# Kernel optimization log

Measured on AMD Instinct MI355X. Metric: run time of the kernel, lower is better.

The kernel has to match this reference:

```python
import jax, jax.numpy as jnp
import numpy as np

T, B, I, H = 512, 64, 1024, 1024
G = 4 * H + 1  # 4 LSTM gates + 1 boundary gate (HM-LSTM)
STDV = 1.0 / np.sqrt(H)


def setup_inputs() -> dict:
    key = jax.random.key(0)
    ks = jax.random.split(key, 5)
    u = lambda k, shape: jax.random.uniform(k, shape, jnp.float32, -STDV, STDV)
    return {
        "x": jax.random.normal(ks[0], (T, B, I), jnp.float32),
        "W_ih": u(ks[1], (G, I)),
        "W_hh": u(ks[2], (G, H)),
        "b_ih": u(ks[3], (G,)),
        "b_hh": u(ks[4], (G,)),
    }


def reference(x, W_ih, W_hh, b_ih, b_hh):
    h_dim = W_hh.shape[1]
    # Precompute input contribution for all timesteps in one big GEMM: [T,B,G]
    gx_all = jnp.einsum("tbi,gi->tbg", x, W_ih) + b_ih + b_hh
    Bsz = x.shape[1]
    h0 = jnp.zeros((Bsz, h_dim), x.dtype)
    c0 = jnp.zeros((Bsz, h_dim), x.dtype)

    def step(carry, gx):
        h, c = carry
        g = gx + h @ W_hh.T  # [B, 4H+1]
        i = jax.nn.sigmoid(g[:, :h_dim])
        f = jax.nn.sigmoid(g[:, h_dim:2 * h_dim])
        gg = jnp.tanh(g[:, 2 * h_dim:3 * h_dim])
        o = jax.nn.sigmoid(g[:, 3 * h_dim:4 * h_dim])
        z = jax.nn.sigmoid(g[:, 4 * h_dim:])  # [B,1] boundary gate
        ig = i * gg
        # HM-LSTM soft boundary: FLUSH (c=i*g) when z->1, UPDATE otherwise
        c_new = z * ig + (1.0 - z) * (f * c + ig)
        h_new = o * jnp.tanh(c_new)
        return (h_new, c_new), h_new

    (hT, cT), out = jax.lax.scan(step, (h0, c0), gx_all)
    return out, hT, cT
```

## Files before the change

kernel.cpp:

```cpp
#include <hip/hip_runtime.h>
#include <cstdint>
#include <cstddef>

typedef unsigned short u16;
typedef short bf16x8 __attribute__((ext_vector_type(8)));
typedef u16   u16x8  __attribute__((ext_vector_type(8)));
typedef float f32x4  __attribute__((ext_vector_type(4)));

#define NT  512
#define NB  64
#define NH  1024
#define NTB 32768
#define G4  4096

#define AS1C(p) ((const __attribute__((address_space(1))) void*)(p))
#define AS3(p)  ((__attribute__((address_space(3))) void*)(p))

__device__ __forceinline__ float b2f(u16 u){
  return __uint_as_float(((unsigned)u) << 16);
}
__device__ __forceinline__ u16 f2b(float f){
  unsigned u = __float_as_uint(f);
  return (u16)((u + 0x7fffu + ((u >> 16) & 1u)) >> 16);
}

__global__ void cvt_bf16(const float* __restrict__ in, u16* __restrict__ out, int n8){
  int stride = gridDim.x * blockDim.x;
  for (int i = blockIdx.x * blockDim.x + threadIdx.x; i < n8; i += stride){
    const float4* p = (const float4*)(in + (size_t)i * 8);
    float4 a = p[0], b = p[1];
    u16x8 r;
    r[0]=f2b(a.x); r[1]=f2b(a.y); r[2]=f2b(a.z); r[3]=f2b(a.w);
    r[4]=f2b(b.x); r[5]=f2b(b.y); r[6]=f2b(b.z); r[7]=f2b(b.w);
    *(u16x8*)(out + (size_t)i * 8) = r;
  }
}

__global__ void zpre_kernel(const float* __restrict__ x, const float* __restrict__ Wih,
                            const float* __restrict__ b_ih, const float* __restrict__ b_hh,
                            float* __restrict__ zp){
  int gw   = (blockIdx.x * 256 + threadIdx.x) >> 6;
  int lane = threadIdx.x & 63;
  const float* wz = Wih + (size_t)4096 * 1024;
  float4 wv[4];
  #pragma unroll
  for (int j = 0; j < 4; ++j) wv[j] = *(const float4*)&wz[lane*16 + j*4];
  float bz = b_ih[4096] + b_hh[4096];
  for (int r = gw; r < NTB; r += 1024){
    const float* xr = x + (size_t)r * 1024 + lane * 16;
    float s = 0.f;
    #pragma unroll
    for (int j = 0; j < 4; ++j){
      float4 xv = *(const float4*)&xr[j*4];
      s += xv.x*wv[j].x + xv.y*wv[j].y + xv.z*wv[j].z + xv.w*wv[j].w;
    }
    #pragma unroll
    for (int o = 32; o > 0; o >>= 1) s += __shfl_down(s, o);
    if (lane == 0) zp[r] = s + bz;
  }
}

template<typename GT>
__global__ __launch_bounds__(256, 2) void gemm_gx(
    const u16* __restrict__ Xb, const u16* __restrict__ Wb,
    const float* __restrict__ b_ih, const float* __restrict__ b_hh,
    GT* __restrict__ gx)
{
  __shared__ u16 As[128*32];
  __shared__ u16 Bs[128*32];
  const int tid  = threadIdx.x;
  const int lane = tid & 63, wave = tid >> 6;
  const int wr = wave >> 1, wc = wave & 1;
  const int m0 = (blockIdx.x & 255) * 128;
  const int n0 = (blockIdx.x >> 8) * 128;
  const int srow = wave * 16 + (lane >> 2);
  const int scol = (lane & 3) * 8;
  const u16* gA = Xb + (size_t)(m0 + srow) * 1024 + scol;
  const u16* gB = Wb + (size_t)(n0 + srow) * 1024 + scol;
  char* lA = (char*)As + wave * 1024;
  char* lB = (char*)Bs + wave * 1024;
  const int fr = lane & 15, fo = (lane >> 4) * 8;

  f32x4 acc[4][4] = {};
  for (int k0 = 0; k0 < 1024; k0 += 32){
    __syncthreads();
    __builtin_amdgcn_global_load_lds(AS1C(gA + k0),            AS3(lA),        16, 0, 0);
    __builtin_amdgcn_global_load_lds(AS1C(gA + 64*1024 + k0),  AS3(lA + 4096), 16, 0, 0);
    __builtin_amdgcn_global_load_lds(AS1C(gB + k0),            AS3(lB),        16, 0, 0);
    __builtin_amdgcn_global_load_lds(AS1C(gB + 64*1024 + k0),  AS3(lB + 4096), 16, 0, 0);
    __syncthreads();
    bf16x8 a[4], b[4];
    #pragma unroll
    for (int mi = 0; mi < 4; ++mi)
      a[mi] = *(const bf16x8*)&As[(wr*64 + mi*16 + fr)*32 + fo];
    #pragma unroll
    for (int ni = 0; ni < 4; ++ni)
      b[ni] = *(const bf16x8*)&Bs[(wc*64 + ni*16 + fr)*32 + fo];
    #pragma unroll
    for (int mi = 0; mi < 4; ++mi)
      #pragma unroll
      for (int ni = 0; ni < 4; ++ni)
        acc[mi][ni] = __builtin_amdgcn_mfma_f32_16x16x32_bf16(a[mi], b[ni], acc[mi][ni], 0, 0, 0);
  }
  const int orow = (lane >> 4) * 4, ocol = lane & 15;
  #pragma unroll
  for (int ni = 0; ni < 4; ++ni){
    const int g = n0 + wc*64 + ni*16 + ocol;
    const float bias = b_ih[g] + b_hh[g];
    #pragma unroll
    for (int mi = 0; mi < 4; ++mi){
      const size_t rb = (size_t)(m0 + wr*64 + mi*16 + orow);
      #pragma unroll
      for (int r = 0; r < 4; ++r){
        float v = acc[mi][ni][r] + bias;
        if constexpr (sizeof(GT) == 4)
          __builtin_nontemporal_store(v, (float*)gx + (rb + r)*G4 + g);
        else
          __builtin_nontemporal_store(f2b(v), (u16*)gx + (rb + r)*G4 + g);
      }
    }
  }
}

__device__ __forceinline__ float ld_gx(const float* p){ return __builtin_nontemporal_load(p); }
__device__ __forceinline__ float ld_gx(const u16* p){ return b2f(__builtin_nontemporal_load(p)); }

template<typename GT>
__global__ __launch_bounds__(256, 1) void hmlstm_scan(
    const u16* __restrict__ Whh, const GT* __restrict__ gx,
    const float* __restrict__ zpre, u16* __restrict__ h0, u16* __restrict__ h1,
    float* __restrict__ out, unsigned* __restrict__ bar)
{
  const int tid  = threadIdx.x;
  const int lane = tid & 63, wave = tid >> 6;
  const int wg = blockIdx.x;
  const int mb = wg >> 6, hb = wg & 63;
  const int fr = lane & 15, hi4 = lane >> 4;
  const int b_l = tid >> 4, h_l = tid & 15;
  const int browg = mb*16 + b_l;

  __shared__ u16  hs[16*1024];
  __shared__ float glds[4][16][16];
  __shared__ float zpart[4][16];
  __shared__ u16  wz[1024];

  ((unsigned long long*)wz)[tid] = ((const unsigned long long*)(Whh + (size_t)4096*1024))[tid];

  const int grow = wave*1024 + hb*16 + fr;
  bf16x8 Bw[32];
  #pragma unroll
  for (int kc = 0; kc < 32; ++kc)
    Bw[kc] = *(const bf16x8*)&Whh[(size_t)grow*1024 + kc*32 + hi4*8];
  #pragma unroll
  for (int kc = 0; kc < 32; ++kc)
    asm volatile("" : "+v"(Bw[kc]));

  {
    u16* p = h0 + (size_t)mb*16384 + hb*256 + tid;
    unsigned z = 0;
    asm volatile("global_store_short %0, %1, off sc0 sc1" :: "v"(p), "v"(z) : "memory");
    asm volatile("s_waitcnt vmcnt(0)" ::: "memory");
  }
  __syncthreads();
  unsigned* myflag = bar + mb*64 + hb;
  const unsigned* gflags = bar + mb*64;
  if (tid == 0){
    unsigned one = 1;
    asm volatile("global_store_dword %0, %1, off sc0 sc1" :: "v"(myflag), "v"(one) : "memory");
  }

  float c_reg = 0.f;

  for (int t = 0; t < NT; ++t){
    const u16* hc = (t & 1) ? h1 : h0;
    u16*       hn = (t & 1) ? h0 : h1;

    float gxl[4];
    const GT* gp = gx + ((size_t)t*64 + mb*16 + hi4*4)*G4 + wave*1024 + hb*16 + fr;
    #pragma unroll
    for (int r = 0; r < 4; ++r) gxl[r] = ld_gx(gp + (size_t)r*G4);
    float zpc = zpre[t*64 + browg];

    {
      const unsigned* fp = gflags + lane;
      unsigned fv, tgt = (unsigned)(t + 1);
      do {
        asm volatile("global_load_dword %0, %1, off sc0 sc1\n\ts_waitcnt vmcnt(0)"
                     : "=v"(fv) : "v"(fp) : "memory");
      } while (!__all((int)(fv >= tgt)));
      __builtin_amdgcn_sched_barrier(0);
    }

    uint4 sv[8];
    #pragma unroll
    for (int j = 0; j < 8; ++j){
      int idx = tid + j*256;
      int row = idx >> 7, cc = idx & 127;
      const u16* src = hc + (size_t)(mb*16 + row)*1024 + cc*8;
      asm volatile("global_load_dwordx4 %0, %1, off sc0 sc1" : "=v"(sv[j]) : "v"(src) : "memory");
    }
    asm volatile("s_waitcnt vmcnt(0)" ::: "memory");
    __builtin_amdgcn_sched_barrier(0);
    #pragma unroll
    for (int j = 0; j < 8; ++j){
      int idx = tid + j*256;
      int row = idx >> 7, cc = idx & 127;
      *(uint4*)((char*)hs + row*2048 + ((cc*16) ^ ((row&7)<<4))) = sv[j];
    }
    __syncthreads();

    f32x4 acc[4] = {}, az = {};
    #pragma unroll
    for (int kc = 0; kc < 32; ++kc){
      bf16x8 a = *(const bf16x8*)((char*)hs + fr*2048 + ((kc*64 + hi4*16) ^ ((fr&7)<<4)));
      acc[kc & 3] = __builtin_amdgcn_mfma_f32_16x16x32_bf16(a, Bw[kc], acc[kc & 3], 0, 0, 0);
    }
    #pragma unroll
    for (int q = 0; q < 8; ++q){
      int kcz = wave*8 + q;
      bf16x8 a  = *(const bf16x8*)((char*)hs + fr*2048 + ((kcz*64 + hi4*16) ^ ((fr&7)<<4)));
      bf16x8 bz = *(const bf16x8*)&wz[kcz*32 + hi4*8];
      az = __builtin_amdgcn_mfma_f32_16x16x32_bf16(a, bz, az, 0, 0, 0);
    }
    f32x4 ac = (acc[0] + acc[1]) + (acc[2] + acc[3]);

    #pragma unroll
    for (int r = 0; r < 4; ++r){
      float v = ac[r] + gxl[r];
      float s = (wave == 2) ? (2.f/(1.f + __expf(-2.f*v)) - 1.f)
                            : (1.f/(1.f + __expf(-v)));
      glds[wave][hi4*4 + r][fr] = s;
    }
    if (fr == 0){
      #pragma unroll
      for (int r = 0; r < 4; ++r) zpart[wave][hi4*4 + r] = az[r];
    }
    __syncthreads();

    float iv = glds[0][b_l][h_l], fvg = glds[1][b_l][h_l];
    float gv = glds[2][b_l][h_l], ov = glds[3][b_l][h_l];
    float zs = zpart[0][b_l] + zpart[1][b_l] + zpart[2][b_l] + zpart[3][b_l];
    float zv = 1.f/(1.f + __expf(-(zpc + zs)));
    float ig = iv * gv;
    float cn = zv*ig + (1.f - zv)*(fvg*c_reg + ig);
    float th = 2.f/(1.f + __expf(-2.f*cn)) - 1.f;
    float hv_ = ov * th;
    c_reg = cn;
    const int hoff = browg*1024 + hb*16 + h_l;
    {
      unsigned hv16 = (unsigned)f2b(hv_);
      asm volatile("global_store_short %0, %1, off sc0 sc1" :: "v"(hn + hoff), "v"(hv16) : "memory");
    }
    __builtin_nontemporal_store(hv_, out + (size_t)t*65536 + hoff);
    if (t == NT-1){
      out[(size_t)NT*65536 + hoff] = hv_;
      out[(size_t)NT*65536 + 65536 + hoff] = cn;
    }
    asm volatile("s_waitcnt vmcnt(0)" ::: "memory");
    __syncthreads();
    if (tid == 0){
      unsigned pv = (unsigned)(t + 2);
      asm volatile("global_store_dword %0, %1, off sc0 sc1" :: "v"(myflag), "v"(pv) : "memory");
    }
  }
}

extern "C" void kernel_launch(void* const* d_in, const int* in_sizes, int n_in,
                              void* d_out, int out_size, void* d_ws, size_t ws_size,
                              hipStream_t stream)
{
  (void)in_sizes; (void)n_in; (void)out_size;
  const float* x    = (const float*)d_in[0];
  const float* Wih  = (const float*)d_in[1];
  const float* Whh  = (const float*)d_in[2];
  const float* b_ih = (const float*)d_in[3];
  const float* b_hh = (const float*)d_in[4];
  float* out = (float*)d_out;

  size_t off = 0;
  auto alloc = [&](size_t bytes)->void*{
    void* p = (char*)d_ws + off;
    off = (off + bytes + 255) & ~(size_t)255;
    return p;
  };
  u16*  xb   = (u16*) alloc((size_t)NTB*1024*2);
  u16*  wihb = (u16*) alloc((size_t)4097*1024*2);
  u16*  whhb = (u16*) alloc((size_t)4097*1024*2);
  u16*  hb   = (u16*) alloc((size_t)2*65536*2);
  float* zp  = (float*)alloc((size_t)NTB*4);
  unsigned* bar = (unsigned*)alloc(4096);
  bool g32 = (ws_size >= off + (size_t)NTB*G4*4);
  void* gxp = (char*)d_ws + off;

  hipMemsetAsync(bar, 0, 4096, stream);
  cvt_bf16<<<dim3(2048), dim3(256), 0, stream>>>(x,   xb,   NTB*1024/8);
  cvt_bf16<<<dim3(512),  dim3(256), 0, stream>>>(Wih, wihb, 4097*1024/8);
  cvt_bf16<<<dim3(512),  dim3(256), 0, stream>>>(Whh, whhb, 4097*1024/8);
  zpre_kernel<<<dim3(256), dim3(256), 0, stream>>>(x, Wih, b_ih, b_hh, zp);
  if (g32){
    gemm_gx<float><<<dim3(8192), dim3(256), 0, stream>>>(xb, wihb, b_ih, b_hh, (float*)gxp);
    hmlstm_scan<float><<<dim3(256), dim3(256), 0, stream>>>(whhb, (const float*)gxp, zp,
                                                            hb, hb + 65536, out, bar);
  } else {
    gemm_gx<u16><<<dim3(8192), dim3(256), 0, stream>>>(xb, wihb, b_ih, b_hh, (u16*)gxp);
    hmlstm_scan<u16><<<dim3(256), dim3(256), 0, stream>>>(whhb, (const u16*)gxp, zp,
                                                          hb, hb + 65536, out, bar);
  }
}
```

Measured before the change: 3.274 ms.

## Use per-wave flags, unique h buffers per step, and direct global-to-LDS loads

```diff
diff --git a/kernel.cpp b/kernel.cpp
--- a/kernel.cpp
+++ b/kernel.cpp
@@ -22,6 +22,12 @@
 __device__ __forceinline__ u16 f2b(float f){
   unsigned u = __float_as_uint(f);
   return (u16)((u + 0x7fffu + ((u >> 16) & 1u)) >> 16);
+}
+__device__ __forceinline__ float fsigmoid(float x){
+  return __builtin_amdgcn_rcpf(1.f + __builtin_amdgcn_exp2f(-1.442695041f * x));
+}
+__device__ __forceinline__ float ftanh(float x){
+  return 2.f * __builtin_amdgcn_rcpf(1.f + __builtin_amdgcn_exp2f(-2.885390082f * x)) - 1.f;
 }
 
 __global__ void cvt_bf16(const float* __restrict__ in, u16* __restrict__ out, int n8){
@@ -128,7 +134,7 @@
 template<typename GT>
 __global__ __launch_bounds__(256, 1) void hmlstm_scan(
     const u16* __restrict__ Whh, const GT* __restrict__ gx,
-    const float* __restrict__ zpre, u16* __restrict__ h0, u16* __restrict__ h1,
+    const float* __restrict__ zpre, u16* __restrict__ hbase,
     float* __restrict__ out, unsigned* __restrict__ bar)
 {
   const int tid  = threadIdx.x;
@@ -156,15 +162,14 @@
     asm volatile("" : "+v"(Bw[kc]));
 
   {
-    u16* p = h0 + (size_t)mb*16384 + hb*256 + tid;
+    u16* p = hbase + (size_t)mb*16384 + hb*256 + tid;
     unsigned z = 0;
     asm volatile("global_store_short %0, %1, off sc0 sc1" :: "v"(p), "v"(z) : "memory");
     asm volatile("s_waitcnt vmcnt(0)" ::: "memory");
   }
-  __syncthreads();
-  unsigned* myflag = bar + mb*64 + hb;
-  const unsigned* gflags = bar + mb*64;
-  if (tid == 0){
+  unsigned* myflag = bar + mb*256 + hb*4 + wave;
+  const unsigned* gflags = bar + mb*256;
+  if (lane == 0){
     unsigned one = 1;
     asm volatile("global_store_dword %0, %1, off sc0 sc1" :: "v"(myflag), "v"(one) : "memory");
   }
@@ -172,8 +177,8 @@
   float c_reg = 0.f;
 
   for (int t = 0; t < NT; ++t){
-    const u16* hc = (t & 1) ? h1 : h0;
-    u16*       hn = (t & 1) ? h0 : h1;
+    const u16* hc = hbase + (size_t)t * 65536;
+    u16*       hn = hbase + (size_t)(t + 1) * 65536;
 
     float gxl[4];
     const GT* gp = gx + ((size_t)t*64 + mb*16 + hi4*4)*G4 + wave*1024 + hb*16 + fr;
@@ -182,31 +187,31 @@
     float zpc = zpre[t*64 + browg];
 
     {
-      const unsigned* fp = gflags + lane;
-      unsigned fv, tgt = (unsigned)(t + 1);
+      const unsigned* fp = gflags + lane*4;
+      unsigned tgt = (unsigned)(t + 1);
+      uint4 fv;
+      unsigned mn;
       do {
-        asm volatile("global_load_dword %0, %1, off sc0 sc1\n\ts_waitcnt vmcnt(0)"
+        asm volatile("global_load_dwordx4 %0, %1, off sc0 sc1\n\ts_waitcnt vmcnt(0)"
                      : "=v"(fv) : "v"(fp) : "memory");
-      } while (!__all((int)(fv >= tgt)));
+        mn = min(min(fv.x, fv.y), min(fv.z, fv.w));
+      } while (!__all((int)(mn >= tgt)));
       __builtin_amdgcn_sched_barrier(0);
     }
 
-    uint4 sv[8];
-    #pragma unroll
-    for (int j = 0; j < 8; ++j){
-      int idx = tid + j*256;
-      int row = idx >> 7, cc = idx & 127;
-      const u16* src = hc + (size_t)(mb*16 + row)*1024 + cc*8;
-      asm volatile("global_load_dwordx4 %0, %1, off sc0 sc1" : "=v"(sv[j]) : "v"(src) : "memory");
+    {
+      const char* gsrc = (const char*)hc + (size_t)mb * 32768;
+      char* hsB = (char*)hs;
+      #pragma unroll
+      for (int j = 0; j < 8; ++j){
+        int chunk = wave*8 + j;
+        int row   = chunk >> 1;
+        int srcoff = row*2048 + ((((chunk & 1)*64 + lane)*16) ^ ((row & 7) << 4));
+        __builtin_amdgcn_global_load_lds(AS1C(gsrc + srcoff), AS3(hsB + chunk*1024), 16, 0, 0);
+      }
     }
     asm volatile("s_waitcnt vmcnt(0)" ::: "memory");
     __builtin_amdgcn_sched_barrier(0);
-    #pragma unroll
-    for (int j = 0; j < 8; ++j){
-      int idx = tid + j*256;
-      int row = idx >> 7, cc = idx & 127;
-      *(uint4*)((char*)hs + row*2048 + ((cc*16) ^ ((row&7)<<4))) = sv[j];
-    }
     __syncthreads();
 
     f32x4 acc[4] = {}, az = {};
@@ -227,8 +232,7 @@
     #pragma unroll
     for (int r = 0; r < 4; ++r){
       float v = ac[r] + gxl[r];
-      float s = (wave == 2) ? (2.f/(1.f + __expf(-2.f*v)) - 1.f)
-                            : (1.f/(1.f + __expf(-v)));
+      float s = (wave == 2) ? ftanh(v) : fsigmoid(v);
       glds[wave][hi4*4 + r][fr] = s;
     }
     if (fr == 0){
@@ -240,27 +244,27 @@
     float iv = glds[0][b_l][h_l], fvg = glds[1][b_l][h_l];
     float gv = glds[2][b_l][h_l], ov = glds[3][b_l][h_l];
     float zs = zpart[0][b_l] + zpart[1][b_l] + zpart[2][b_l] + zpart[3][b_l];
-    float zv = 1.f/(1.f + __expf(-(zpc + zs)));
+    float zv = fsigmoid(zpc + zs);
     float ig = iv * gv;
     float cn = zv*ig + (1.f - zv)*(fvg*c_reg + ig);
-    float th = 2.f/(1.f + __expf(-2.f*cn)) - 1.f;
-    float hv_ = ov * th;
+    float hv_ = ov * ftanh(cn);
     c_reg = cn;
     const int hoff = browg*1024 + hb*16 + h_l;
+
     {
       unsigned hv16 = (unsigned)f2b(hv_);
       asm volatile("global_store_short %0, %1, off sc0 sc1" :: "v"(hn + hoff), "v"(hv16) : "memory");
-    }
+      asm volatile("s_waitcnt vmcnt(0)" ::: "memory");
+      if (lane == 0){
+        unsigned pv = (unsigned)(t + 2);
+        asm volatile("global_store_dword %0, %1, off sc0 sc1" :: "v"(myflag), "v"(pv) : "memory");
+      }
+    }
+
     __builtin_nontemporal_store(hv_, out + (size_t)t*65536 + hoff);
     if (t == NT-1){
       out[(size_t)NT*65536 + hoff] = hv_;
       out[(size_t)NT*65536 + 65536 + hoff] = cn;
-    }
-    asm volatile("s_waitcnt vmcnt(0)" ::: "memory");
-    __syncthreads();
-    if (tid == 0){
-      unsigned pv = (unsigned)(t + 2);
-      asm volatile("global_store_dword %0, %1, off sc0 sc1" :: "v"(myflag), "v"(pv) : "memory");
     }
   }
 }
@@ -283,11 +287,11 @@
     off = (off + bytes + 255) & ~(size_t)255;
     return p;
   };
-  u16*  xb   = (u16*) alloc((size_t)NTB*1024*2);
-  u16*  wihb = (u16*) alloc((size_t)4097*1024*2);
-  u16*  whhb = (u16*) alloc((size_t)4097*1024*2);
-  u16*  hb   = (u16*) alloc((size_t)2*65536*2);
-  float* zp  = (float*)alloc((size_t)NTB*4);
+  u16*  xb    = (u16*) alloc((size_t)NTB*1024*2);
+  u16*  wihb  = (u16*) alloc((size_t)4097*1024*2);
+  u16*  whhb  = (u16*) alloc((size_t)4097*1024*2);
+  u16*  hbase = (u16*) alloc((size_t)(NT+1)*65536*2);
+  float* zp   = (float*)alloc((size_t)NTB*4);
   unsigned* bar = (unsigned*)alloc(4096);
   bool g32 = (ws_size >= off + (size_t)NTB*G4*4);
   void* gxp = (char*)d_ws + off;
@@ -300,10 +304,10 @@
   if (g32){
     gemm_gx<float><<<dim3(8192), dim3(256), 0, stream>>>(xb, wihb, b_ih, b_hh, (float*)gxp);
     hmlstm_scan<float><<<dim3(256), dim3(256), 0, stream>>>(whhb, (const float*)gxp, zp,
-                                                            hb, hb + 65536, out, bar);
+                                                            hbase, out, bar);
   } else {
     gemm_gx<u16><<<dim3(8192), dim3(256), 0, stream>>>(xb, wihb, b_ih, b_hh, (u16*)gxp);
     hmlstm_scan<u16><<<dim3(256), dim3(256), 0, stream>>>(whhb, (const u16*)gxp, zp,
-                                                          hb, hb + 65536, out, bar);
-  }
-}
+                                                          hbase, out, bar);
+  }
+}
```

Result: slower. 3.902 ms (+19.2%).
